# Kernel optimization log

Measured on AMD Instinct MI355X. Metric: run time of the kernel, lower is better.

Reference implementation:

```python
import jax, jax.numpy as jnp
import numpy as np

B = 256
N_VERTS = 10475
N_JOINTS = 55  # 1 root + 21 body + jaw + 2 eyes + 2*15 hands
NUM_BETAS = 10
NUM_EXPR = 10
POSE_BASIS = (N_JOINTS - 1) * 9  # 486
# SMPL-X kinematic tree (parent index per joint, root = -1)
PARENTS = np.array([-1,0,0,0,1,2,3,4,5,6,7,8,9,9,9,12,13,14,16,17,18,19,15,15,15,
                    20,25,26,20,28,29,20,31,32,20,34,35,20,37,38,
                    21,40,41,21,43,44,21,46,47,21,49,50,21,52,53], dtype=np.int64)


def _rodrigues(aa):
    # axis-angle [..., 3] -> rotation matrix [..., 3, 3]
    angle = jnp.linalg.norm(aa, axis=-1, keepdims=True) + 1e-8
    axis = aa / angle
    x, y, z = axis[..., 0], axis[..., 1], axis[..., 2]
    zero = jnp.zeros_like(x)
    K = jnp.stack([zero, -z, y, z, zero, -x, -y, x, zero], axis=-1).reshape(aa.shape[:-1] + (3, 3))
    s = jnp.sin(angle)[..., None]
    c = jnp.cos(angle)[..., None]
    I = jnp.eye(3, dtype=aa.dtype)
    return I + s * K + (1.0 - c) * (K @ K)


def setup_inputs() -> dict:
    key = jax.random.key(0)
    ks = jax.random.split(key, 16)
    def rots(k, nj, scale=0.2):
        aa = jax.random.normal(k, (B, nj, 3), dtype=jnp.float32) * scale
        return _rodrigues(aa)
    inp = {
        'world_rot': rots(ks[0], 1, 0.5),
        'world_tsl': jax.random.normal(ks[1], (B, 3), dtype=jnp.float32),
        'body_shape': jax.random.normal(ks[2], (B, NUM_BETAS), dtype=jnp.float32),
        'body_pose': rots(ks[3], 21),
        'left_hand_pose': rots(ks[4], 15),
        'right_hand_pose': rots(ks[5], 15),
        'expr_shape': jax.random.normal(ks[6], (B, NUM_EXPR), dtype=jnp.float32),
        'jaw_pose': rots(ks[7], 1),
        'leye_pose': rots(ks[8], 1),
        'reye_pose': rots(ks[9], 1),
        # model buffers (synthetic, SMPL-X-sized)
        'v_template': jax.random.normal(ks[10], (N_VERTS, 3), dtype=jnp.float32) * 0.3,
        'shapedirs': jax.random.normal(ks[11], (N_VERTS, 3, NUM_BETAS), dtype=jnp.float32) * 0.01,
        'expr_dirs': jax.random.normal(ks[12], (N_VERTS, 3, NUM_EXPR), dtype=jnp.float32) * 0.01,
        'posedirs': jax.random.normal(ks[13], (POSE_BASIS, N_VERTS * 3), dtype=jnp.float32) * 0.01,
        'J_regressor': jax.nn.softmax(jax.random.normal(ks[14], (N_JOINTS, N_VERTS), dtype=jnp.float32) * 4.0, axis=-1),
        'lbs_weights': jax.nn.softmax(jax.random.normal(ks[15], (N_VERTS, N_JOINTS), dtype=jnp.float32) * 4.0, axis=-1),
    }
    return inp


def _lbs(world_rot, world_tsl, body_shape, body_pose, left_hand_pose, right_hand_pose,
         expr_shape, jaw_pose, leye_pose, reye_pose,
         v_template, shapedirs, expr_dirs, posedirs, J_regressor, lbs_weights):
    dtype = v_template.dtype
    # full pose: [B, 55, 3, 3]
    full_pose = jnp.concatenate([world_rot, body_pose, jaw_pose, leye_pose, reye_pose,
                                 left_hand_pose, right_hand_pose], axis=1)
    b = full_pose.shape[0]
    # shape + expression blendshapes
    v_shaped = v_template[None] + jnp.einsum('bk,nck->bnc', body_shape, shapedirs) \
               + jnp.einsum('bk,nck->bnc', expr_shape, expr_dirs)
    # rest-pose joints [B, J, 3]
    joints = jnp.einsum('jn,bnc->bjc', J_regressor, v_shaped)
    # pose blendshapes
    ident = jnp.eye(3, dtype=dtype)
    pose_feature = (full_pose[:, 1:] - ident).reshape(b, POSE_BASIS)
    v_posed = v_shaped + (pose_feature @ posedirs).reshape(b, N_VERTS, 3)
    # relative joint locations w.r.t. parent
    rel_joints = joints.at[:, 1:].add(-joints[:, PARENTS[1:]])
    # local 4x4 transforms [B, J, 4, 4]
    top = jnp.concatenate([full_pose, rel_joints[..., None]], axis=-1)  # [B,J,3,4]
    bottom = jnp.broadcast_to(jnp.array([0., 0., 0., 1.], dtype=dtype), (b, N_JOINTS, 1, 4))
    T = jnp.concatenate([top, bottom], axis=2)
    # kinematic chain recurrence (small fixed joint count -> unrolled)
    chain = [T[:, 0]]
    for i in range(1, N_JOINTS):
        chain.append(chain[PARENTS[i]] @ T[:, i])
    A = jnp.stack(chain, axis=1)  # [B, J, 4, 4]
    posed_joints = A[..., :3, 3]
    # remove rest-pose joint offset so A maps rest -> posed
    t_corr = posed_joints - jnp.einsum('bjkl,bjl->bjk', A[..., :3, :3], joints)
    A_rel = A.at[..., :3, 3].set(t_corr)
    # linear blend skinning: per-vertex transform [B, N, 4, 4]
    T_vert = jnp.einsum('nj,bjkl->bnkl', lbs_weights, A_rel)
    verts = jnp.einsum('bnkl,bnl->bnk', T_vert[..., :3, :3], v_posed) + T_vert[..., :3, 3]
    verts = verts + world_tsl[:, None]
    joints_out = posed_joints + world_tsl[:, None]
    return verts, joints_out


def reference(world_rot, world_tsl, body_shape, body_pose, left_hand_pose, right_hand_pose,
              expr_shape, jaw_pose, leye_pose, reye_pose,
              v_template, shapedirs, expr_dirs, posedirs, J_regressor, lbs_weights):
    return _lbs(world_rot, world_tsl, body_shape, body_pose, left_hand_pose, right_hand_pose,
                expr_shape, jaw_pose, leye_pose, reye_pose,
                v_template, shapedirs, expr_dirs, posedirs, J_regressor, lbs_weights)
```

## Files before the change

kernel.cpp:

```cpp
#include <hip/hip_runtime.h>
#include <stdint.h>

#define BATCH 256
#define NV 10475
#define NVP 10496
#define NJ 55
#define PB 486
#define KS 506
#define VC (NV*3)
#define KP 512
#define BKC 32
#define NCHUNK 16
#define BN 64
#define JCH 8
#define JCHUNK 1312

typedef short bf16x8 __attribute__((ext_vector_type(8)));
typedef float f32x4  __attribute__((ext_vector_type(4)));

__constant__ int c_parents[NJ] = {
  -1,0,0,0,1,2,3,4,5,6,7,8,9,9,9,12,13,14,16,17,18,19,15,15,15,
  20,25,26,20,28,29,20,31,32,20,34,35,20,37,38,21,40,41,21,43,44,
  21,46,47,21,49,50,21,52,53};

__constant__ int c_depth[NJ] = {
  0,1,1,1,2,2,2,3,3,3,4,4,4,4,4,5,5,5,6,6,7,7,6,6,6,
  8,9,10,8,9,10,8,9,10,8,9,10,8,9,10,
  8,9,10,8,9,10,8,9,10,8,9,10,8,9,10};

__device__ __forceinline__ unsigned short f2bf(float x){
  uint32_t u = __float_as_uint(x);
  uint32_t r = (u + 0x7fffu + ((u >> 16) & 1u)) >> 16;
  return (unsigned short)r;
}
__device__ __forceinline__ float bf2f(unsigned short h){
  return __uint_as_float(((uint32_t)h) << 16);
}

__global__ __launch_bounds__(256) void k_prep(
    const float* __restrict__ lw, const float* __restrict__ sd,
    const float* __restrict__ ed, unsigned short* __restrict__ lwb,
    float* __restrict__ sdedT) {
  int bid = blockIdx.x;
  const int LWB_BLOCKS = (NVP*64)/256;
  if (bid < LWB_BLOCKS) {
    int idx = bid*256 + threadIdx.x;
    int n = idx >> 6, j = idx & 63;
    float v = (n < NV && j < NJ) ? lw[(size_t)n*NJ + j] : 0.f;
    unsigned short hi = f2bf(v);
    float lo = v - bf2f(hi);
    lwb[idx] = hi;
    lwb[(size_t)NVP*64 + idx] = f2bf(lo);
  } else {
    int idx = (bid - LWB_BLOCKS)*256 + threadIdx.x;
    if (idx >= 20*VC) return;
    int r = idx / VC, col = idx - r*VC;
    int n = col/3, c = col - n*3;
    float v = (r < 10) ? sd[(size_t)n*30 + c*10 + r]
                       : ed[(size_t)n*30 + c*10 + (r-10)];
    sdedT[idx] = v;
  }
}

__device__ __forceinline__ const float* pose_src(int j, int b,
    const float* wrot, const float* bpose, const float* jaw, const float* leye,
    const float* reye, const float* lhand, const float* rhand) {
  if (j==0)  return wrot  + b*9;
  if (j<=21) return bpose + (b*21 + (j-1))*9;
  if (j==22) return jaw   + b*9;
  if (j==23) return leye  + b*9;
  if (j==24) return reye  + b*9;
  if (j<=39) return lhand + (b*15 + (j-25))*9;
  return rhand + (b*15 + (j-40))*9;
}

__global__ __launch_bounds__(512) void k_posefeat(
    const float* __restrict__ bpose, const float* __restrict__ jaw,
    const float* __restrict__ leye, const float* __restrict__ reye,
    const float* __restrict__ lhand, const float* __restrict__ rhand,
    const float* __restrict__ bs, const float* __restrict__ es,
    unsigned short* __restrict__ pfb) {
  int b = blockIdx.x, t = threadIdx.x;
  unsigned short o = 0;
  if (t < PB){
    int jj = t/9, rc = t - jj*9;
    const float* rs = pose_src(jj+1, b, nullptr, bpose, jaw, leye, reye, lhand, rhand);
    float v = rs[rc];
    if (rc==0 || rc==4 || rc==8) v -= 1.0f;
    o = f2bf(v);
  } else if (t < 496){
    o = f2bf(bs[b*10 + (t-486)]);
  } else if (t < KS){
    o = f2bf(es[b*10 + (t-496)]);
  }
  pfb[(size_t)b*KP + t] = o;
}

__global__ __launch_bounds__(256) void k_jsmall(
    const float* __restrict__ jreg, const float* __restrict__ sd,
    const float* __restrict__ ed, const float* __restrict__ vt,
    float* __restrict__ part) {
  int ch = blockIdx.x, j = blockIdx.y;
  int t = threadIdx.x;
  float acc[63];
  #pragma unroll
  for (int s=0;s<63;s++) acc[s]=0.f;
  int n0 = ch*JCHUNK, nend = min(n0+JCHUNK, NV);
  for (int n = n0 + t; n < nend; n += 256){
    float w = jreg[(size_t)j*NV + n];
    const float* sp = sd + (size_t)n*30;
    const float* ep = ed + (size_t)n*30;
    const float* vp = vt + (size_t)n*3;
    #pragma unroll
    for (int c=0;c<3;c++){
      #pragma unroll
      for (int q=0;q<10;q++){
        acc[c*21+q]    += w*sp[c*10+q];
        acc[c*21+10+q] += w*ep[c*10+q];
      }
      acc[c*21+20] += w*vp[c];
    }
  }
  #pragma unroll
  for (int s=0;s<63;s++){
    float a = acc[s];
    #pragma unroll
    for (int d=32; d>=1; d>>=1) a += __shfl_xor(a,d);
    acc[s]=a;
  }
  __shared__ float red[4][63];
  int w = t>>6, l = t&63;
  if (l==0){
    #pragma unroll
    for (int s=0;s<63;s++) red[w][s]=acc[s];
  }
  __syncthreads();
  if (t < 63){
    float a = red[0][t]+red[1][t]+red[2][t]+red[3][t];
    part[((size_t)j*JCH+ch)*63 + t] = a;
  }
}

__global__ __launch_bounds__(192) void k_joints2(
    const float* __restrict__ part, const float* __restrict__ bs,
    const float* __restrict__ es, float* __restrict__ joints) {
  int b = blockIdx.x, t = threadIdx.x;
  if (t >= NJ*3) return;
  int j = t/3, c = t - j*3;
  float S[21];
  #pragma unroll
  for (int q=0;q<21;q++) S[q]=0.f;
  for (int ch=0; ch<JCH; ch++){
    const float* p = part + ((size_t)j*JCH+ch)*63 + c*21;
    #pragma unroll
    for (int q=0;q<21;q++) S[q] += p[q];
  }
  float a = S[20];
  #pragma unroll
  for (int q=0;q<10;q++) a += S[q]*bs[b*10+q] + S[10+q]*es[b*10+q];
  joints[(size_t)b*NJ*3 + t] = a;
}

__global__ __launch_bounds__(256) void k_chain(
    const float* __restrict__ wrot, const float* __restrict__ bpose,
    const float* __restrict__ jaw, const float* __restrict__ leye,
    const float* __restrict__ reye, const float* __restrict__ lhand,
    const float* __restrict__ rhand, const float* __restrict__ wtsl,
    const float* __restrict__ joints,
    unsigned short* __restrict__ arelb, float* __restrict__ jout) {
  const int w = threadIdx.x >> 6, lane = threadIdx.x & 63;
  const int b = blockIdx.x*4 + w;
  const int j = lane;
  const bool act = (j < NJ);

  float R[9] = {1.f,0.f,0.f, 0.f,1.f,0.f, 0.f,0.f,1.f};
  if (act){
    const float* rs = pose_src(j, b, wrot, bpose, jaw, leye, reye, lhand, rhand);
    #pragma unroll
    for (int i=0;i<9;i++) R[i]=rs[i];
  }
  float jx=0.f, jy=0.f, jz=0.f;
  if (act){
    const float* jb = joints + (size_t)b*NJ*3 + j*3;
    jx=jb[0]; jy=jb[1]; jz=jb[2];
  }
  int par = act ? c_parents[j] : 0;
  if (par < 0) par = 0;
  float px = __shfl(jx, par), py = __shfl(jy, par), pz = __shfl(jz, par);
  float t0, t1, t2;
  if (j == 0){ t0=jx; t1=jy; t2=jz; }
  else       { t0=jx-px; t1=jy-py; t2=jz-pz; }

  float M[12];
  #pragma unroll
  for (int r=0;r<3;r++){
    M[r*4+0]=R[r*3+0]; M[r*4+1]=R[r*3+1]; M[r*4+2]=R[r*3+2]; M[r*4+3]= (r==0?t0:(r==1?t1:t2));
  }
  int dep = act ? c_depth[j] : 99;

  #pragma unroll
  for (int L=1; L<=10; L++){
    float pm[12];
    #pragma unroll
    for (int i=0;i<12;i++) pm[i] = __shfl(M[i], par);
    if (dep == L){
      #pragma unroll
      for (int r=0;r<3;r++){
        float p0=pm[r*4+0], p1=pm[r*4+1], p2=pm[r*4+2], p3=pm[r*4+3];
        M[r*4+0] = p0*R[0]+p1*R[3]+p2*R[6];
        M[r*4+1] = p0*R[1]+p1*R[4]+p2*R[7];
        M[r*4+2] = p0*R[2]+p1*R[5]+p2*R[8];
        M[r*4+3] = p0*t0 + p1*t1 + p2*t2 + p3;
      }
    }
  }

  float wx=wtsl[b*3+0], wy=wtsl[b*3+1], wz=wtsl[b*3+2];
  if (act){
    jout[((size_t)b*NJ+j)*3+0] = M[3]  + wx;
    jout[((size_t)b*NJ+j)*3+1] = M[7]  + wy;
    jout[((size_t)b*NJ+j)*3+2] = M[11] + wz;
  }
  float A[12];
  #pragma unroll
  for (int r=0;r<3;r++){
    A[r*4+0]=M[r*4+0]; A[r*4+1]=M[r*4+1]; A[r*4+2]=M[r*4+2];
    A[r*4+3]=M[r*4+3] - (M[r*4+0]*jx + M[r*4+1]*jy + M[r*4+2]*jz);
  }
  unsigned short* ah = arelb + (size_t)(b*2+0)*16*64;
  unsigned short* al = arelb + (size_t)(b*2+1)*16*64;
  #pragma unroll
  for (int e=0;e<16;e++){
    float v = (e < 12 && act) ? A[e] : 0.f;
    unsigned short hi = f2bf(v);
    float lo = v - bf2f(hi);
    ah[e*64 + j] = hi;
    al[e*64 + j] = f2bf(lo);
  }
}

__global__ __launch_bounds__(256) void k_vposed(
    const float* __restrict__ pd, const float* __restrict__ sdedT,
    const float* __restrict__ vt, const unsigned short* __restrict__ pfb,
    float* __restrict__ vsh) {
  __shared__ __align__(16) unsigned short sB[2][BN*40];
  const int tid  = threadIdx.x;
  const int w    = tid >> 6, lane = tid & 63;
  const int m16  = lane & 15, quad = lane >> 4;
  const int col0 = blockIdx.x * BN;

  f32x4 acc[4][4];
  #pragma unroll
  for (int i=0;i<4;i++)
    #pragma unroll
    for (int j=0;j<4;j++) acc[i][j] = (f32x4){0.f,0.f,0.f,0.f};

  #pragma unroll
  for (int i=0;i<8;i++){
    int idx = tid + i*256;
    int k = idx >> 6, n = idx & 63;
    int cc = col0 + n;
    float v = (cc < VC) ? pd[(size_t)k*VC + cc] : 0.f;
    sB[0][n*40 + k] = f2bf(v);
  }

  for (int c=0; c<NCHUNK; c++){
    __syncthreads();
    const unsigned short* sBc = sB[c&1];
    const int k0 = c*BKC;
    bf16x8 a[4], bb[4];
    #pragma unroll
    for (int mi=0;mi<4;mi++){
      int row = w*64 + mi*16 + m16;
      a[mi] = *((const bf16x8*)(pfb + (size_t)row*KP + k0 + quad*8));
    }
    #pragma unroll
    for (int ni=0;ni<4;ni++)
      bb[ni] = *((const bf16x8*)(sBc + (ni*16 + m16)*40 + quad*8));
    #pragma unroll
    for (int mi=0;mi<4;mi++)
      #pragma unroll
      for (int ni=0;ni<4;ni++)
        acc[mi][ni] = __builtin_amdgcn_mfma_f32_16x16x32_bf16(
                          a[mi], bb[ni], acc[mi][ni], 0, 0, 0);
    if (c+1 < NCHUNK){
      unsigned short* sBn = sB[(c+1)&1];
      const int k0n = (c+1)*BKC;
      #pragma unroll
      for (int i=0;i<8;i++){
        int idx = tid + i*256;
        int k = idx >> 6, n = idx & 63;
        int kk = k0n + k, cc = col0 + n;
        float v = 0.f;
        if (cc < VC){
          if (kk < PB)      v = pd[(size_t)kk*VC + cc];
          else if (kk < KS) v = sdedT[(size_t)(kk-PB)*VC + cc];
        }
        sBn[n*40 + k] = f2bf(v);
      }
    }
  }
  #pragma unroll
  for (int mi=0;mi<4;mi++){
    int rbase = w*64 + mi*16 + quad*4;
    #pragma unroll
    for (int ni=0;ni<4;ni++){
      int col = col0 + ni*16 + m16;
      if (col < VC){
        float vtc = vt[col];
        #pragma unroll
        for (int r=0;r<4;r++)
          vsh[(size_t)(rbase + r)*VC + col] = acc[mi][ni][r] + vtc;
      }
    }
  }
}

__global__ __launch_bounds__(256) void k_verts(
    const unsigned short* __restrict__ lwb, const unsigned short* __restrict__ arelb,
    const float* __restrict__ wtsl, float* __restrict__ out) {
  __shared__ float sT[16*64*17];
  const int tid = threadIdx.x, w = tid >> 6, lane = tid & 63;
  const int m16 = lane & 15, quad = lane >> 4;
  const int n0 = blockIdx.x*64;
  const int b0 = blockIdx.y*16;

  bf16x8 ahh[4][2], all[4][2];
  #pragma unroll
  for (int t4=0;t4<4;t4++){
    int row = n0 + t4*16 + m16;
    #pragma unroll
    for (int kc=0;kc<2;kc++){
      ahh[t4][kc] = *((const bf16x8*)(lwb + (size_t)row*64 + kc*32 + quad*8));
      all[t4][kc] = *((const bf16x8*)(lwb + (size_t)NVP*64 + (size_t)row*64 + kc*32 + quad*8));
    }
  }
  for (int bi=0; bi<4; bi++){
    int b = b0 + w*4 + bi;
    bf16x8 bh[2], bl[2];
    #pragma unroll
    for (int kc=0;kc<2;kc++){
      bh[kc] = *((const bf16x8*)(arelb + ((size_t)(b*2+0)*16 + m16)*64 + kc*32 + quad*8));
      bl[kc] = *((const bf16x8*)(arelb + ((size_t)(b*2+1)*16 + m16)*64 + kc*32 + quad*8));
    }
    f32x4 acc[4];
    #pragma unroll
    for (int t4=0;t4<4;t4++) acc[t4] = (f32x4){0.f,0.f,0.f,0.f};
    #pragma unroll
    for (int t4=0;t4<4;t4++)
      #pragma unroll
      for (int kc=0;kc<2;kc++){
        acc[t4] = __builtin_amdgcn_mfma_f32_16x16x32_bf16(ahh[t4][kc], bh[kc], acc[t4], 0,0,0);
        acc[t4] = __builtin_amdgcn_mfma_f32_16x16x32_bf16(all[t4][kc], bh[kc], acc[t4], 0,0,0);
        acc[t4] = __builtin_amdgcn_mfma_f32_16x16x32_bf16(ahh[t4][kc], bl[kc], acc[t4], 0,0,0);
      }
    if (m16 < 12){
      int slot = w*4 + bi;
      #pragma unroll
      for (int t4=0;t4<4;t4++){
        #pragma unroll
        for (int r=0;r<4;r++){
          int vert = t4*16 + quad*4 + r;
          sT[(slot*64 + vert)*17 + m16] = acc[t4][r];
        }
      }
    }
  }
  __syncthreads();
  #pragma unroll
  for (int it=0; it<4; it++){
    int pid = it*256 + tid;
    int bb = pid >> 6, v = pid & 63;
    int n = n0 + v;
    if (n >= NV) continue;
    int b = b0 + bb;
    const float* Tp = &sT[(bb*64 + v)*17];
    float T[12];
    #pragma unroll
    for (int e=0;e<12;e++) T[e] = Tp[e];
    float* op = out + ((size_t)b*NV + n)*3;
    float x=op[0], y=op[1], z=op[2];
    float tx=wtsl[b*3+0], ty=wtsl[b*3+1], tz=wtsl[b*3+2];
    op[0] = T[0]*x + T[1]*y + T[2] *z + T[3]  + tx;
    op[1] = T[4]*x + T[5]*y + T[6] *z + T[7]  + ty;
    op[2] = T[8]*x + T[9]*y + T[10]*z + T[11] + tz;
  }
}

extern "C" void kernel_launch(void* const* d_in, const int* in_sizes, int n_in,
                              void* d_out, int out_size, void* d_ws, size_t ws_size,
                              hipStream_t stream) {
  const float* wrot   = (const float*)d_in[0];
  const float* wtsl   = (const float*)d_in[1];
  const float* bshape = (const float*)d_in[2];
  const float* bpose  = (const float*)d_in[3];
  const float* lhand  = (const float*)d_in[4];
  const float* rhand  = (const float*)d_in[5];
  const float* eshape = (const float*)d_in[6];
  const float* jaw    = (const float*)d_in[7];
  const float* leye   = (const float*)d_in[8];
  const float* reye   = (const float*)d_in[9];
  const float* vt     = (const float*)d_in[10];
  const float* sd     = (const float*)d_in[11];
  const float* ed     = (const float*)d_in[12];
  const float* pd     = (const float*)d_in[13];
  const float* jreg   = (const float*)d_in[14];
  const float* lw     = (const float*)d_in[15];
  float* out = (float*)d_out;

  float* vsh  = out;
  float* jout = out + (size_t)BATCH*NV*3;

  float* ws     = (float*)d_ws;
  float* joints = ws;
  float* part   = joints + (size_t)BATCH*NJ*3;
  float* sdedT  = part   + (size_t)NJ*JCH*63;
  unsigned short* pfb   = (unsigned short*)(sdedT + (size_t)20*VC);
  unsigned short* lwb   = pfb + (size_t)BATCH*KP;
  unsigned short* arelb = lwb + (size_t)2*NVP*64;

  const int PREP_BLOCKS = (NVP*64)/256 + (20*VC + 255)/256;

  k_prep    <<<PREP_BLOCKS, 256, 0, stream>>>(lw, sd, ed, lwb, sdedT);
  k_posefeat<<<BATCH, 512, 0, stream>>>(bpose, jaw, leye, reye, lhand, rhand,
                                        bshape, eshape, pfb);
  k_jsmall  <<<dim3(JCH, NJ), 256, 0, stream>>>(jreg, sd, ed, vt, part);
  k_joints2 <<<BATCH, 192, 0, stream>>>(part, bshape, eshape, joints);
  k_chain   <<<64, 256, 0, stream>>>(wrot, bpose, jaw, leye, reye, lhand, rhand,
                                     wtsl, joints, arelb, jout);
  k_vposed  <<<(VC+BN-1)/BN, 256, 0, stream>>>(pd, sdedT, vt, pfb, vsh);
  k_verts   <<<dim3(NVP/64, 16), 256, 0, stream>>>(lwb, arelb, wtsl, out);
}
```

Measured before the change: 271.1 us.

## Load pose-basis B fragments directly from global memory, dropping LDS staging

The posedirs GEMM kernel no longer stages B tiles through a double-buffered shared-memory array. Each lane now gathers its own bf16 B fragment straight from global memory, so the per-chunk __syncthreads goes away, and the last K chunk is peeled off to handle the shapedirs/expr rows. Launch bounds now request two blocks per SM. The cost is that every B element is loaded by all four waves (4x redundant global traffic), and each lane reads 8 strided K rows per fragment, which coalesces poorly and leans on cache.

```diff
diff --git a/kernel.cpp b/kernel.cpp
--- a/kernel.cpp
+++ b/kernel.cpp
@@ -239,11 +239,10 @@
   }
 }
 
-__global__ __launch_bounds__(256) void k_vposed(
+__global__ __launch_bounds__(256, 2) void k_vposed(
     const float* __restrict__ pd, const float* __restrict__ sdedT,
     const float* __restrict__ vt, const unsigned short* __restrict__ pfb,
     float* __restrict__ vsh) {
-  __shared__ __align__(16) unsigned short sB[2][BN*40];
   const int tid  = threadIdx.x;
   const int w    = tid >> 6, lane = tid & 63;
   const int m16  = lane & 15, quad = lane >> 4;
@@ -255,50 +254,59 @@
     #pragma unroll
     for (int j=0;j<4;j++) acc[i][j] = (f32x4){0.f,0.f,0.f,0.f};
 
-  #pragma unroll
-  for (int i=0;i<8;i++){
-    int idx = tid + i*256;
-    int k = idx >> 6, n = idx & 63;
-    int cc = col0 + n;
-    float v = (cc < VC) ? pd[(size_t)k*VC + cc] : 0.f;
-    sB[0][n*40 + k] = f2bf(v);
-  }
-
-  for (int c=0; c<NCHUNK; c++){
-    __syncthreads();
-    const unsigned short* sBc = sB[c&1];
+  int bcol[4];
+  #pragma unroll
+  for (int ni=0;ni<4;ni++) bcol[ni] = min(col0 + ni*16 + m16, VC-1);
+
+  const unsigned short* pfa = pfb + (size_t)(w*64 + m16)*KP + quad*8;
+
+  #pragma unroll 2
+  for (int c=0; c<15; c++){
     const int k0 = c*BKC;
-    bf16x8 a[4], bb[4];
-    #pragma unroll
-    for (int mi=0;mi<4;mi++){
-      int row = w*64 + mi*16 + m16;
-      a[mi] = *((const bf16x8*)(pfb + (size_t)row*KP + k0 + quad*8));
-    }
-    #pragma unroll
-    for (int ni=0;ni<4;ni++)
-      bb[ni] = *((const bf16x8*)(sBc + (ni*16 + m16)*40 + quad*8));
+    bf16x8 a[4];
+    #pragma unroll
+    for (int mi=0;mi<4;mi++)
+      a[mi] = *((const bf16x8*)(pfa + (size_t)mi*16*KP + k0));
+    union { bf16x8 v; unsigned short s[8]; } bb[4];
+    #pragma unroll
+    for (int ni=0;ni<4;ni++){
+      #pragma unroll
+      for (int j=0;j<8;j++){
+        int kk = k0 + quad*8 + j;
+        bb[ni].s[j] = f2bf(pd[(size_t)kk*VC + bcol[ni]]);
+      }
+    }
     #pragma unroll
     for (int mi=0;mi<4;mi++)
       #pragma unroll
       for (int ni=0;ni<4;ni++)
         acc[mi][ni] = __builtin_amdgcn_mfma_f32_16x16x32_bf16(
-                          a[mi], bb[ni], acc[mi][ni], 0, 0, 0);
-    if (c+1 < NCHUNK){
-      unsigned short* sBn = sB[(c+1)&1];
-      const int k0n = (c+1)*BKC;
-      #pragma unroll
-      for (int i=0;i<8;i++){
-        int idx = tid + i*256;
-        int k = idx >> 6, n = idx & 63;
-        int kk = k0n + k, cc = col0 + n;
-        float v = 0.f;
-        if (cc < VC){
-          if (kk < PB)      v = pd[(size_t)kk*VC + cc];
-          else if (kk < KS) v = sdedT[(size_t)(kk-PB)*VC + cc];
-        }
-        sBn[n*40 + k] = f2bf(v);
-      }
-    }
+                          a[mi], bb[ni].v, acc[mi][ni], 0, 0, 0);
+  }
+  {
+    const int k0 = 15*BKC;
+    bf16x8 a[4];
+    #pragma unroll
+    for (int mi=0;mi<4;mi++)
+      a[mi] = *((const bf16x8*)(pfa + (size_t)mi*16*KP + k0));
+    union { bf16x8 v; unsigned short s[8]; } bb[4];
+    #pragma unroll
+    for (int ni=0;ni<4;ni++){
+      #pragma unroll
+      for (int j=0;j<8;j++){
+        int kk = k0 + quad*8 + j;
+        float f = 0.f;
+        if (kk < PB)      f = pd[(size_t)kk*VC + bcol[ni]];
+        else if (kk < KS) f = sdedT[(size_t)(kk-PB)*VC + bcol[ni]];
+        bb[ni].s[j] = f2bf(f);
+      }
+    }
+    #pragma unroll
+    for (int mi=0;mi<4;mi++)
+      #pragma unroll
+      for (int ni=0;ni<4;ni++)
+        acc[mi][ni] = __builtin_amdgcn_mfma_f32_16x16x32_bf16(
+                          a[mi], bb[ni].v, acc[mi][ni], 0, 0, 0);
   }
   #pragma unroll
   for (int mi=0;mi<4;mi++){
```

New measurement: 255.4 us. 1.06x faster.
